# Kernel optimization log

Measured on AMD Instinct MI355X. Metric: run time of the kernel, lower is better.

The kernel has to match this reference:

```python
import jax, jax.numpy as jnp
import numpy as np

B, T, C, H = 8, 1024, 768, 12
D = C // H  # head dim = 64

def setup_inputs() -> dict:
    key = jax.random.key(0)
    k0, k1, k2, k3, k4 = jax.random.split(key, 5)
    x = jax.random.normal(k0, (B, T, C), dtype=jnp.float32)
    # flax Dense params: kernel [in, out], bias [out]
    c_attn_kernel = jax.random.normal(k1, (C, 3 * C), dtype=jnp.float32) * (1.0 / np.sqrt(C))
    c_attn_bias = jax.random.normal(k2, (3 * C,), dtype=jnp.float32) * 0.01
    c_proj_kernel = jax.random.normal(k3, (C, C), dtype=jnp.float32) * (1.0 / np.sqrt(C))
    c_proj_bias = jax.random.normal(k4, (C,), dtype=jnp.float32) * 0.01
    return {"x": x, "c_attn_kernel": c_attn_kernel, "c_attn_bias": c_attn_bias,
            "c_proj_kernel": c_proj_kernel, "c_proj_bias": c_proj_bias}

def reference(x, c_attn_kernel, c_attn_bias, c_proj_kernel, c_proj_bias):
    Bc, Tc, Cc = x.shape
    qkv = x @ c_attn_kernel + c_attn_bias          # [B, T, 3C]
    q, k, v = jnp.split(qkv, 3, axis=-1)
    q = q.reshape(Bc, Tc, H, D).swapaxes(1, 2)     # [B, H, T, D]
    k = k.reshape(Bc, Tc, H, D).swapaxes(1, 2)
    v = v.reshape(Bc, Tc, H, D).swapaxes(1, 2)
    att = jnp.matmul(q, k.swapaxes(-2, -1)) * (1.0 / jnp.sqrt(jnp.float32(D)))  # [B, H, T, T]
    mask = jnp.tril(jnp.ones((Tc, Tc), dtype=bool)).reshape(1, 1, Tc, Tc)
    att = jnp.where(mask, att, -jnp.inf)
    att = jax.nn.softmax(att, axis=-1)
    # dropout=0.0 / train=False -> identity
    y = jnp.matmul(att, v)                          # [B, H, T, D]
    y = y.swapaxes(1, 2).reshape(Bc, Tc, Cc)        # [B, T, C]
    y = y @ c_proj_kernel + c_proj_bias
    return y
```

## Files before the change

kernel.cpp:

```cpp
#include <hip/hip_runtime.h>
#include <hip/hip_bf16.h>
#include <math.h>

#define BATCH 8
#define SEQ   1024
#define CH    768
#define NH    12
#define HD    64
#define HSZ   (BATCH * NH * SEQ * HD)

typedef __attribute__((ext_vector_type(8))) short short8;
typedef __attribute__((ext_vector_type(4))) short short4v;
typedef __attribute__((ext_vector_type(4))) float floatx4;

static __device__ inline short f2bf(float f) {
    union { float f; unsigned u; } x; x.f = f;
    unsigned r = (x.u + 0x7fffu + ((x.u >> 16) & 1u)) >> 16;
    return (short)r;
}

#define GLOAD_LDS16(g, l)                                                     \
    __builtin_amdgcn_global_load_lds(                                         \
        (const __attribute__((address_space(1))) void*)(g),                   \
        (__attribute__((address_space(3))) void*)(l), 16, 0, 0)

#define NCAST (BATCH * SEQ * CH / 1024)
#define NTA   ((3 * CH / 32) * (CH / 32))
#define NTP   ((CH / 32) * (CH / 32))

__device__ __forceinline__ void transpose_tile(
    const float* __restrict__ w, short* __restrict__ wt, int K, int N,
    int bx, int by, int tid, float (*tile)[33])
{
    const int tx = tid & 31, ty = tid >> 5;
    const int n0 = bx * 32, k0 = by * 32;
    #pragma unroll
    for (int i = 0; i < 4; i++)
        tile[ty + i * 8][tx] = w[(size_t)(k0 + ty + i * 8) * N + n0 + tx];
    __syncthreads();
    #pragma unroll
    for (int i = 0; i < 4; i++)
        wt[(size_t)(n0 + ty + i * 8) * K + k0 + tx] = f2bf(tile[tx][ty + i * 8]);
}

__global__ __launch_bounds__(256) void prep_kernel(
    const float* __restrict__ x, short* __restrict__ xb,
    const float* __restrict__ wa, short* __restrict__ wta,
    const float* __restrict__ wp, short* __restrict__ wtp)
{
    __shared__ float tile[32][33];
    const int bid = blockIdx.x, tid = threadIdx.x;
    if (bid < NCAST) {
        int i = (bid * 256 + tid) * 4;
        float4 v = *(const float4*)(x + i);
        short4v o = { f2bf(v.x), f2bf(v.y), f2bf(v.z), f2bf(v.w) };
        *(short4v*)(xb + i) = o;
    } else if (bid < NCAST + NTA) {
        int t = bid - NCAST;
        transpose_tile(wa, wta, CH, 3 * CH, t % (3 * CH / 32), t / (3 * CH / 32), tid, tile);
    } else {
        int t = bid - NCAST - NTA;
        transpose_tile(wp, wtp, CH, CH, t % (CH / 32), t / (CH / 32), tid, tile);
    }
}

template <int MODE, int BM, int BN, int NBLK, int MBX, int WPE>
__global__ __launch_bounds__(256, WPE) void gemm_bt_kernel(
    const short* __restrict__ A, const short* __restrict__ Bt,
    const float* __restrict__ bias, void* __restrict__ outv,
    int M, int N, int K)
{
    constexpr int MT  = BM / 32;
    constexpr int NT  = BN / 32;
    constexpr int ACH = BM / 64;
    constexpr int BCH = BN / 64;
    constexpr int STAGE_BYTES = (BM + BN) * 128;
    constexpr int EPI_BYTES   = (MODE == 1) ? (BN * 136 * 2) : 0;
    constexpr int LDS_BYTES   = STAGE_BYTES > EPI_BYTES ? STAGE_BYTES : EPI_BYTES;
    __shared__ __align__(16) char smem[LDS_BYTES];
    short* AsB = (short*)smem;
    short* BsB = (short*)(smem + BM * 128);

    const int tid  = threadIdx.x;
    const int lane = tid & 63;
    const int col  = lane & 15;
    const int quad = lane >> 4;
    const int wave = tid >> 6;
    const int wm = wave & 1, wn = wave >> 1;

    const int bid = blockIdx.x;
    const int j   = bid & 7;
    const int t   = bid >> 3;
    const int mb  = j * MBX + t / NBLK;
    const int nb  = t % NBLK;
    const int m0 = mb * BM, n0 = nb * BN;

    const int srow = tid >> 2;
    const int kc   = ((tid & 3) ^ (srow & 3)) * 8;
    const short* aptr[ACH];
    const short* bptr[BCH];
    #pragma unroll
    for (int c = 0; c < ACH; c++)
        aptr[c] = A + (size_t)(m0 + c * 64 + srow) * K + kc;
    #pragma unroll
    for (int c = 0; c < BCH; c++)
        bptr[c] = Bt + (size_t)(n0 + c * 64 + srow) * K + kc;

    floatx4 acc[MT][NT];
    #pragma unroll
    for (int i = 0; i < MT; i++)
        #pragma unroll
        for (int jj = 0; jj < NT; jj++)
            acc[i][jj] = (floatx4){0.f, 0.f, 0.f, 0.f};

    const int niter = K / 32;

    #pragma unroll
    for (int c = 0; c < ACH; c++) GLOAD_LDS16(aptr[c], &AsB[c * 2048 + tid * 8]);
    #pragma unroll
    for (int c = 0; c < BCH; c++) GLOAD_LDS16(bptr[c], &BsB[c * 2048 + tid * 8]);

    for (int k = 0; k < niter; k++) {
        __syncthreads();
        const int cur = k & 1, nxt = cur ^ 1;
        if (k + 1 < niter) {
            const int ko = (k + 1) * 32;
            #pragma unroll
            for (int c = 0; c < ACH; c++)
                GLOAD_LDS16(aptr[c] + ko, &AsB[nxt * BM * 32 + c * 2048 + tid * 8]);
            #pragma unroll
            for (int c = 0; c < BCH; c++)
                GLOAD_LDS16(bptr[c] + ko, &BsB[nxt * BN * 32 + c * 2048 + tid * 8]);
        }
        short8 af[MT], bf[NT];
        #pragma unroll
        for (int mt = 0; mt < MT; mt++) {
            const int row = wm * (BM / 2) + mt * 16 + col;
            af[mt] = *(const short8*)&AsB[cur * BM * 32 + row * 32 + ((quad ^ (row & 3)) << 3)];
        }
        #pragma unroll
        for (int nt = 0; nt < NT; nt++) {
            const int row = wn * (BN / 2) + nt * 16 + col;
            bf[nt] = *(const short8*)&BsB[cur * BN * 32 + row * 32 + ((quad ^ (row & 3)) << 3)];
        }
        #pragma unroll
        for (int mt = 0; mt < MT; mt++)
            #pragma unroll
            for (int nt = 0; nt < NT; nt++)
                acc[mt][nt] = __builtin_amdgcn_mfma_f32_16x16x32_bf16(
                    af[mt], bf[nt], acc[mt][nt], 0, 0, 0);
    }

    if constexpr (MODE == 0) {
        #pragma unroll
        for (int mt = 0; mt < MT; mt++) {
            #pragma unroll
            for (int r = 0; r < 4; r++) {
                const int m = m0 + wm * (BM / 2) + mt * 16 + quad * 4 + r;
                #pragma unroll
                for (int nt = 0; nt < NT; nt++) {
                    const int n = n0 + wn * (BN / 2) + nt * 16 + col;
                    ((float*)outv)[(size_t)m * N + n] = acc[mt][nt][r] + bias[n];
                }
            }
        }
    } else {
        __syncthreads();
        short* Es = (short*)smem;
        const int sel = n0 / CH;
        const int h0  = (n0 - sel * CH) >> 6;
        const int bb  = m0 >> 10;
        const int t0  = m0 & 1023;
        short* qkv = (short*)outv;

        if (sel < 2) {
            #pragma unroll
            for (int mt = 0; mt < MT; mt++)
                #pragma unroll
                for (int r = 0; r < 4; r++) {
                    const int lm = wm * (BM / 2) + mt * 16 + quad * 4 + r;
                    #pragma unroll
                    for (int nt = 0; nt < NT; nt++) {
                        const int ln = wn * (BN / 2) + nt * 16 + col;
                        Es[lm * 200 + ln] = f2bf(acc[mt][nt][r] + bias[n0 + ln]);
                    }
                }
            __syncthreads();
            #pragma unroll
            for (int it = 0; it < (BM * BN / 8) / 256; it++) {
                const int id = it * 256 + tid;
                const int hp = id >> 10, lm = (id >> 3) & 127, dc = id & 7;
                short8 v = *(const short8*)&Es[lm * 200 + hp * 64 + dc * 8];
                size_t dst = (size_t)sel * HSZ +
                    (((size_t)(bb * NH + h0 + hp)) * SEQ + t0 + lm) * HD + dc * 8;
                *(short8*)&qkv[dst] = v;
            }
        } else {
            #pragma unroll
            for (int nt = 0; nt < NT; nt++) {
                const int ln = wn * (BN / 2) + nt * 16 + col;
                const float bv = bias[n0 + ln];
                #pragma unroll
                for (int mt = 0; mt < MT; mt++) {
                    const int lm = wm * (BM / 2) + mt * 16 + quad * 4;
                    short4v pk;
                    #pragma unroll
                    for (int r = 0; r < 4; r++) pk[r] = f2bf(acc[mt][nt][r] + bv);
                    *(short4v*)&Es[ln * 136 + lm] = pk;
                }
            }
            __syncthreads();
            #pragma unroll
            for (int it = 0; it < (BM * BN / 8) / 256; it++) {
                const int id = it * 256 + tid;
                const int ln = id >> 4, tc = id & 15;
                short8 v = *(const short8*)&Es[ln * 136 + tc * 8];
                const int hp = ln >> 6, d = ln & 63;
                size_t dst = (size_t)2 * HSZ +
                    (((size_t)(bb * NH + h0 + hp)) * HD + d) * SEQ + t0 + tc * 8;
                *(short8*)&qkv[dst] = v;
            }
        }
    }
}

#define LDK 72

template <bool DIAG>
__device__ __forceinline__ void strip_step(
    const short* __restrict__ Ksh, const short* __restrict__ Vsh,
    short* __restrict__ pw, const short8* aq, floatx4* acc_o,
    floatx4& lacc, short8 bones, int col, int quad, int qrow0)
{
    floatx4 sacc[4];
    #pragma unroll
    for (int i = 0; i < 4; i++) sacc[i] = (floatx4){0.f, 0.f, 0.f, 0.f};
    #pragma unroll
    for (int s = 0; s < 2; s++)
        #pragma unroll
        for (int nt = 0; nt < 4; nt++) {
            short8 bk = *(const short8*)&Ksh[(nt * 16 + col) * LDK + s * 32 + quad * 8];
            sacc[nt] = __builtin_amdgcn_mfma_f32_16x16x32_bf16(aq[s], bk, sacc[nt], 0, 0, 0);
        }

    const float SCL = 0.18033688011112042f;
    #pragma unroll
    for (int r = 0; r < 4; r++)
        #pragma unroll
        for (int nt = 0; nt < 4; nt++) {
            float sv = sacc[nt][r] * SCL;
            if (DIAG && (nt * 16 + col) > (qrow0 + r)) sv = -INFINITY;
            float pv = __builtin_amdgcn_exp2f(sv);
            pw[(quad * 4 + r) * LDK + nt * 16 + col] =
                (short)(__builtin_bit_cast(unsigned, pv) >> 16);
        }
    __builtin_amdgcn_wave_barrier();

    short8 ap[2];
    ap[0] = *(const short8*)&pw[col * LDK + quad * 8];
    ap[1] = *(const short8*)&pw[col * LDK + 32 + quad * 8];

    #pragma unroll
    for (int s = 0; s < 2; s++) {
        #pragma unroll
        for (int nt = 0; nt < 4; nt++) {
            short8 bv = *(const short8*)&Vsh[(nt * 16 + col) * LDK + s * 32 + quad * 8];
            acc_o[nt] = __builtin_amdgcn_mfma_f32_16x16x32_bf16(ap[s], bv, acc_o[nt], 0, 0, 0);
        }
        lacc = __builtin_amdgcn_mfma_f32_16x16x32_bf16(ap[s], bones, lacc, 0, 0, 0);
    }
}

__global__ __launch_bounds__(256, 3) void attn_kernel(
    const short* __restrict__ Qg, const short* __restrict__ Kg,
    const short* __restrict__ Vg, short* __restrict__ Y)
{
    __shared__ __align__(16) short Ksh[64 * LDK];
    __shared__ __align__(16) short Vsh[64 * LDK];
    __shared__ __align__(16) short Psh[4][2][16 * LDK];

    const int tid  = threadIdx.x;
    const int wave = tid >> 6;
    const int lane = tid & 63;
    const int col  = lane & 15;
    const int quad = lane >> 4;
    const int bh = blockIdx.x;
    const int qt = 7 - blockIdx.y;
    const int b = bh / NH, h = bh - b * NH;

    const size_t kqbase = (size_t)bh * SEQ * HD;
    const size_t vbase  = (size_t)bh * HD * SEQ;

    short8 aq[2][2];
    #pragma unroll
    for (int st = 0; st < 2; st++) {
        const short* qp = Qg + kqbase +
            (size_t)(qt * 128 + st * 64 + wave * 16 + col) * HD + quad * 8;
        aq[st][0] = *(const short8*)(qp);
        aq[st][1] = *(const short8*)(qp + 32);
    }

    floatx4 acc_o[2][4];
    floatx4 lacc[2];
    #pragma unroll
    for (int st = 0; st < 2; st++) {
        lacc[st] = (floatx4){0.f, 0.f, 0.f, 0.f};
        #pragma unroll
        for (int i = 0; i < 4; i++) acc_o[st][i] = (floatx4){0.f, 0.f, 0.f, 0.f};
    }

    const short one_bf = (short)0x3F80;
    short8 bones = (col == 0)
        ? (short8){one_bf, one_bf, one_bf, one_bf, one_bf, one_bf, one_bf, one_bf}
        : (short8){0, 0, 0, 0, 0, 0, 0, 0};

    const int qrow0 = wave * 16 + quad * 4;

    const int idx0 = tid * 8, idx1 = (256 + tid) * 8;
    const int row0 = idx0 >> 6, offs0 = idx0 & 63;
    const int row1 = idx1 >> 6, offs1 = idx1 & 63;

    short8 kreg[2], vreg[2];
    {
        const short* ksrc = Kg + kqbase;
        const short* vsrc = Vg + vbase;
        kreg[0] = *(const short8*)&ksrc[idx0];
        kreg[1] = *(const short8*)&ksrc[idx1];
        vreg[0] = *(const short8*)&vsrc[(size_t)row0 * SEQ + offs0];
        vreg[1] = *(const short8*)&vsrc[(size_t)row1 * SEQ + offs1];
    }

    const int nkt = 2 * qt + 2;
    for (int kt = 0; kt < nkt; kt++) {
        __syncthreads();
        *(short8*)&Ksh[row0 * LDK + offs0] = kreg[0];
        *(short8*)&Ksh[row1 * LDK + offs1] = kreg[1];
        *(short8*)&Vsh[row0 * LDK + offs0] = vreg[0];
        *(short8*)&Vsh[row1 * LDK + offs1] = vreg[1];
        __syncthreads();

        if (kt + 1 < nkt) {
            const short* ksrc = Kg + kqbase + (size_t)(kt + 1) * 64 * HD;
            const short* vsrc = Vg + vbase + (kt + 1) * 64;
            kreg[0] = *(const short8*)&ksrc[idx0];
            kreg[1] = *(const short8*)&ksrc[idx1];
            vreg[0] = *(const short8*)&vsrc[(size_t)row0 * SEQ + offs0];
            vreg[1] = *(const short8*)&vsrc[(size_t)row1 * SEQ + offs1];
        }

        if (kt < 2 * qt) {
            strip_step<false>(Ksh, Vsh, Psh[wave][0], aq[0], acc_o[0], lacc[0],
                              bones, col, quad, qrow0);
            strip_step<false>(Ksh, Vsh, Psh[wave][1], aq[1], acc_o[1], lacc[1],
                              bones, col, quad, qrow0);
        } else if (kt == 2 * qt) {
            strip_step<true>(Ksh, Vsh, Psh[wave][0], aq[0], acc_o[0], lacc[0],
                             bones, col, quad, qrow0);
            strip_step<false>(Ksh, Vsh, Psh[wave][1], aq[1], acc_o[1], lacc[1],
                              bones, col, quad, qrow0);
        } else {
            strip_step<true>(Ksh, Vsh, Psh[wave][1], aq[1], acc_o[1], lacc[1],
                             bones, col, quad, qrow0);
        }
    }

    #pragma unroll
    for (int st = 0; st < 2; st++) {
        #pragma unroll
        for (int r = 0; r < 4; r++) {
            float l = __shfl(lacc[st][r], quad * 16, 64);
            float inv = 1.f / l;
            int t = qt * 128 + st * 64 + wave * 16 + quad * 4 + r;
            size_t ybase = ((size_t)(b * SEQ + t)) * CH + h * HD;
            #pragma unroll
            for (int nt = 0; nt < 4; nt++)
                Y[ybase + nt * 16 + col] = f2bf(acc_o[st][nt][r] * inv);
        }
    }
}

extern "C" void kernel_launch(void* const* d_in, const int* in_sizes, int n_in,
                              void* d_out, int out_size, void* d_ws, size_t ws_size,
                              hipStream_t stream)
{
    const float* x      = (const float*)d_in[0];
    const float* w_attn = (const float*)d_in[1];
    const float* b_attn = (const float*)d_in[2];
    const float* w_proj = (const float*)d_in[3];
    const float* b_proj = (const float*)d_in[4];
    float* out = (float*)d_out;

    short* qkv16 = (short*)d_ws;
    short* y16   = qkv16 + (size_t)3 * HSZ;
    short* xb    = y16   + (size_t)HSZ;
    short* wta   = xb    + (size_t)HSZ;
    short* wtp   = wta   + (size_t)3 * CH * CH;

    const int M = BATCH * SEQ;

    prep_kernel<<<NCAST + NTA + NTP, 256, 0, stream>>>(x, xb, w_attn, wta, w_proj, wtp);

    gemm_bt_kernel<1, 128, 192, 12, 8, 3><<<768, 256, 0, stream>>>(
        xb, wta, b_attn, qkv16, M, 3 * CH, CH);

    dim3 ga(BATCH * NH, SEQ / 128);
    attn_kernel<<<ga, 256, 0, stream>>>(qkv16, qkv16 + (size_t)HSZ,
                                        qkv16 + (size_t)2 * HSZ, y16);

    gemm_bt_kernel<0, 64, 192, 4, 16, 4><<<512, 256, 0, stream>>>(
        y16, wtp, b_proj, out, M, CH, CH);
}
```

Measured before the change: 170.2 us.

## Replace QKV GEMM with 256x192-tile 8-wave double-buffered kernel

Adds a dedicated QKV projection kernel that runs 512 threads (8 waves) per block on 256x192 output tiles. It double-buffers K-slices in LDS through direct global-to-LDS loads and interleaves the prefetch with the MFMA phases, using barriers and s_setprio. Blocks are mapped by XCD so that neighbouring M-tiles share an L2. The epilogue writes Q/K head-major and V transposed through an LDS staging buffer. The larger tiles increase data reuse and cut the block count from 768 to 384, at the cost of higher register and LDS pressure and lower occupancy.

```diff
diff --git a/kernel.cpp b/kernel.cpp
--- a/kernel.cpp
+++ b/kernel.cpp
@@ -23,6 +23,12 @@
     __builtin_amdgcn_global_load_lds(                                         \
         (const __attribute__((address_space(1))) void*)(g),                   \
         (__attribute__((address_space(3))) void*)(l), 16, 0, 0)
+
+#define BARF()  do { asm volatile("" ::: "memory");                           \
+                     __builtin_amdgcn_s_barrier();                            \
+                     asm volatile("" ::: "memory"); } while (0)
+#define LGKM0() asm volatile("s_waitcnt lgkmcnt(0)" ::: "memory")
+#define VMC0()  asm volatile("s_waitcnt vmcnt(0)" ::: "memory")
 
 #define NCAST (BATCH * SEQ * CH / 1024)
 #define NTA   ((3 * CH / 32) * (CH / 32))
@@ -64,6 +70,172 @@
     }
 }
 
+__global__ __launch_bounds__(512, 2) void gemm1_8ph_kernel(
+    const short* __restrict__ A, const short* __restrict__ Bt,
+    const float* __restrict__ bias, short* __restrict__ qkv)
+{
+    const int K = CH;
+    __shared__ __align__(16) short smem[57344];
+    short* As = smem;
+    short* Bs = smem + 32768;
+
+    const int tid  = threadIdx.x;
+    const int lane = tid & 63;
+    const int col  = lane & 15;
+    const int quad = lane >> 4;
+    const int wave = tid >> 6;
+    const int wm   = wave >> 2;
+    const int wn   = wave & 3;
+
+    const int bid = blockIdx.x;
+    const int xcd = bid & 7;
+    const int t8  = bid >> 3;
+    const int mb  = xcd * 4 + t8 / 12;
+    const int nb  = t8 % 12;
+    const int m0  = mb * 256;
+    const int n0  = nb * 192;
+
+    const int srow = tid >> 3;
+    const int swz  = ((tid & 7) ^ (srow & 7)) << 3;
+    const short* aP[4];
+    const short* bP[3];
+    #pragma unroll
+    for (int c = 0; c < 4; ++c)
+        aP[c] = A + (size_t)(m0 + c * 64 + srow) * K + swz;
+    #pragma unroll
+    for (int c = 0; c < 3; ++c)
+        bP[c] = Bt + (size_t)(n0 + c * 64 + srow) * K + swz;
+
+    const int cswz0 = ((quad) ^ (col & 7)) << 3;
+    const int cswz1 = cswz0 ^ 32;
+    const int aBase = (wm * 128 + col) * 64;
+    const int bBase = (wn * 48 + col) * 64;
+
+    floatx4 acc[8][3];
+    #pragma unroll
+    for (int i = 0; i < 8; ++i)
+        #pragma unroll
+        for (int j = 0; j < 3; ++j)
+            acc[i][j] = (floatx4){0.f, 0.f, 0.f, 0.f};
+
+    #pragma unroll
+    for (int c = 0; c < 4; ++c) GLOAD_LDS16(aP[c], &As[c * 4096 + tid * 8]);
+    #pragma unroll
+    for (int c = 0; c < 3; ++c) GLOAD_LDS16(bP[c], &Bs[c * 4096 + tid * 8]);
+    VMC0();
+    BARF();
+
+    #pragma unroll 1
+    for (int t = 0; t < 12; ++t) {
+        const int  P  = t & 1;
+        const bool pf = (t < 11);
+        const int  sk = (t + 1) * 64;
+        const short* lA = As + P * 16384;
+        const short* lB = Bs + P * 12288;
+        short* wA = As + (P ^ 1) * 16384;
+        short* wB = Bs + (P ^ 1) * 12288;
+
+        short8 bf[3][2];
+        #pragma unroll
+        for (int nt = 0; nt < 3; ++nt) {
+            bf[nt][0] = *(const short8*)&lB[bBase + nt * 1024 + cswz0];
+            bf[nt][1] = *(const short8*)&lB[bBase + nt * 1024 + cswz1];
+        }
+
+        #pragma unroll
+        for (int g = 0; g < 4; ++g) {
+            short8 af[2][2];
+            #pragma unroll
+            for (int dm = 0; dm < 2; ++dm) {
+                const int ro = aBase + (g * 2 + dm) * 1024;
+                af[dm][0] = *(const short8*)&lA[ro + cswz0];
+                af[dm][1] = *(const short8*)&lA[ro + cswz1];
+            }
+            if (g == 0 && pf) {
+                #pragma unroll
+                for (int c = 0; c < 4; ++c)
+                    GLOAD_LDS16(aP[c] + sk, &wA[c * 4096 + tid * 8]);
+            }
+            if (g == 1 && pf) {
+                #pragma unroll
+                for (int c = 0; c < 3; ++c)
+                    GLOAD_LDS16(bP[c] + sk, &wB[c * 4096 + tid * 8]);
+            }
+            BARF();
+            LGKM0();
+            __builtin_amdgcn_s_setprio(1);
+            #pragma unroll
+            for (int s = 0; s < 2; ++s)
+                #pragma unroll
+                for (int dm = 0; dm < 2; ++dm)
+                    #pragma unroll
+                    for (int nt = 0; nt < 3; ++nt)
+                        acc[g * 2 + dm][nt] = __builtin_amdgcn_mfma_f32_16x16x32_bf16(
+                            af[dm][s], bf[nt][s], acc[g * 2 + dm][nt], 0, 0, 0);
+            __builtin_amdgcn_s_setprio(0);
+            if (g == 3) VMC0();
+            BARF();
+        }
+    }
+
+    short* Es = smem;
+    const int sel = nb >> 2;
+    const int h0  = (nb & 3) * 3;
+    const int bb  = m0 >> 10;
+    const int t0  = m0 & 1023;
+
+    if (sel < 2) {
+        #pragma unroll
+        for (int nt = 0; nt < 3; ++nt) {
+            const int ln = wn * 48 + nt * 16 + col;
+            const float bv = bias[n0 + ln];
+            #pragma unroll
+            for (int mt = 0; mt < 8; ++mt)
+                #pragma unroll
+                for (int r = 0; r < 4; ++r) {
+                    const int lm = wm * 128 + mt * 16 + quad * 4 + r;
+                    Es[lm * 200 + ln] = f2bf(acc[mt][nt][r] + bv);
+                }
+        }
+        BARF();
+        #pragma unroll
+        for (int it = 0; it < 12; ++it) {
+            const int id = it * 512 + tid;
+            const int lm = id / 24, c24 = id - lm * 24;
+            const int hp = c24 >> 3, dc = c24 & 7;
+            short8 v = *(const short8*)&Es[lm * 200 + hp * 64 + dc * 8];
+            size_t dst = (size_t)sel * HSZ +
+                (((size_t)(bb * NH + h0 + hp)) * SEQ + t0 + lm) * HD + dc * 8;
+            *(short8*)&qkv[dst] = v;
+        }
+    } else {
+        #pragma unroll
+        for (int nt = 0; nt < 3; ++nt) {
+            const int ln = wn * 48 + nt * 16 + col;
+            const float bv = bias[n0 + ln];
+            #pragma unroll
+            for (int mt = 0; mt < 8; ++mt) {
+                const int lm = wm * 128 + mt * 16 + quad * 4;
+                short4v pk;
+                #pragma unroll
+                for (int r = 0; r < 4; ++r) pk[r] = f2bf(acc[mt][nt][r] + bv);
+                *(short4v*)&Es[ln * 264 + lm] = pk;
+            }
+        }
+        BARF();
+        #pragma unroll
+        for (int it = 0; it < 12; ++it) {
+            const int id = it * 512 + tid;
+            const int ln = id >> 5, tc = id & 31;
+            short8 v = *(const short8*)&Es[ln * 264 + tc * 8];
+            const int hp = ln >> 6, d = ln & 63;
+            size_t dst = (size_t)2 * HSZ +
+                (((size_t)(bb * NH + h0 + hp)) * HD + d) * SEQ + t0 + tc * 8;
+            *(short8*)&qkv[dst] = v;
+        }
+    }
+}
+
 template <int MODE, int BM, int BN, int NBLK, int MBX, int WPE>
 __global__ __launch_bounds__(256, WPE) void gemm_bt_kernel(
     const short* __restrict__ A, const short* __restrict__ Bt,
@@ -400,8 +572,7 @@
 
     prep_kernel<<<NCAST + NTA + NTP, 256, 0, stream>>>(x, xb, w_attn, wta, w_proj, wtp);
 
-    gemm_bt_kernel<1, 128, 192, 12, 8, 3><<<768, 256, 0, stream>>>(
-        xb, wta, b_attn, qkv16, M, 3 * CH, CH);
+    gemm1_8ph_kernel<<<384, 512, 0, stream>>>(xb, wta, b_attn, qkv16);
 
     dim3 ga(BATCH * NH, SEQ / 128);
     attn_kernel<<<ga, 256, 0, stream>>>(qkv16, qkv16 + (size_t)HSZ,
```

Result: slower. 175.2 us (+2.9%).
